# Optimization experiments

Hardware: AMD Instinct MI355X
Metric: run time of the kernel (lower is better)

Reference implementation:

```python
import jax, jax.numpy as jnp
import numpy as np

EMBED = 1024
N_HEAD = 16
D_HID = EMBED // N_HEAD
R_FF = 4
D_FF = EMBED * R_FF
LN_EPS = 1e-5


def layer_norm(x, gamma, beta):
    mu = jnp.mean(x, axis=-1, keepdims=True)
    var = jnp.var(x, axis=-1, keepdims=True)
    return (x - mu) * jax.lax.rsqrt(var + LN_EPS) * gamma + beta


def setup_inputs() -> dict:
    key = jax.random.key(0)
    ks = jax.random.split(key, 10)
    B, S = 4, 2048
    # torch nn.Linear stores weight as [out, in]; y = x @ W.T
    def xavier(k, shape):
        fan_out, fan_in = shape
        lim = np.sqrt(6.0 / (fan_in + fan_out))
        return jax.random.uniform(k, shape, jnp.float32, -lim, lim)
    return {
        "x": jax.random.normal(ks[0], (B, S, EMBED), jnp.float32),
        "Wq": xavier(ks[1], (EMBED, EMBED)),
        "Wk": xavier(ks[2], (EMBED, EMBED)),
        "Wv": xavier(ks[3], (EMBED, EMBED)),
        "Wo": xavier(ks[4], (EMBED, EMBED)),
        "bo": jnp.zeros((EMBED,), jnp.float32),
        "ln1_g": jnp.ones((EMBED,), jnp.float32),
        "ln1_b": jnp.zeros((EMBED,), jnp.float32),
        "ln2_g": jnp.ones((EMBED,), jnp.float32),
        "ln2_b": jnp.zeros((EMBED,), jnp.float32),
        "W1": jax.random.normal(ks[5], (D_FF, EMBED), jnp.float32) * np.sqrt(2.0 / EMBED),
        "b1": jnp.zeros((D_FF,), jnp.float32),
        "W2": xavier(ks[6], (EMBED, D_FF)),
        "b2": jnp.zeros((EMBED,), jnp.float32),
    }


def reference(x, Wq, Wk, Wv, Wo, bo, ln1_g, ln1_b, ln2_g, ln2_b, W1, b1, W2, b2):
    B, S, E = x.shape
    scaling = 1.0 / np.sqrt(D_HID)
    # --- attention (pre-LN), dropout = identity (eval) ---
    xn = layer_norm(x, ln1_g, ln1_b)
    q = (xn @ Wq.T).reshape(B, S, N_HEAD, D_HID) * scaling
    k = (xn @ Wk.T).reshape(B, S, N_HEAD, D_HID)
    v = (xn @ Wv.T).reshape(B, S, N_HEAD, D_HID)
    scores = jnp.einsum("bqhd,bkhd->bhqk", q, k)
    attn = jax.nn.softmax(scores, axis=-1)
    out = jnp.einsum("bhqk,bkhd->bqhd", attn, v).reshape(B, S, E)
    out = out @ Wo.T + bo
    x = x + out
    # --- feed-forward (pre-LN) ---
    xn = layer_norm(x, ln2_g, ln2_b)
    h = jax.nn.relu(xn @ W1.T + b1)
    x = x + (h @ W2.T + b2)
    return x
```

## Files before the change

kernel.cpp:

```cpp
#include <hip/hip_runtime.h>
#include <hip/hip_bf16.h>
#include <cstdint>


typedef __attribute__((ext_vector_type(8))) short bf16x8;
typedef __attribute__((ext_vector_type(4))) float f32x4;

#define LDSAS __attribute__((address_space(3)))
#define GLBAS __attribute__((address_space(1)))

#define CQK 0.18033688011112044f

__device__ __forceinline__ unsigned short f2bf(float f) {
  union { float f; unsigned u; } c; c.f = f;
  unsigned u = c.u + 0x7fffu + ((c.u >> 16) & 1u);
  return (unsigned short)(u >> 16);
}

__device__ __forceinline__ unsigned pk2(float a, float b) {
  __hip_bfloat162 h = __float22bfloat162_rn(make_float2(a, b));
  union { __hip_bfloat162 h; unsigned u; } c; c.h = h; return c.u;
}

__device__ __forceinline__ void async16(const unsigned short* g, unsigned short* l) {
  __builtin_amdgcn_global_load_lds((const GLBAS unsigned int*)g,
                                   (LDSAS unsigned int*)l, 16, 0, 0);
}

__global__ void cvt_all(const float* __restrict__ q, const float* __restrict__ k,
                        const float* __restrict__ v, const float* __restrict__ o,
                        const float* __restrict__ w1, const float* __restrict__ w2,
                        unsigned short* __restrict__ wsb) {
  const long i = (long)blockIdx.x * 256 + threadIdx.x;
  const float* src; unsigned short* dst; long off;
  if (i < 1048576) {
    const long seg = i >> 18, o4 = i & 262143;
    src = (seg == 0) ? q : (seg == 1) ? k : (seg == 2) ? v : o;
    dst = wsb + ((seg == 3) ? 3145728L : seg * 1048576L);
    off = o4;
  } else if (i < 2097152) {
    src = w1; dst = wsb + 4194304; off = i - 1048576;
  } else {
    src = w2; dst = wsb + 8388608; off = i - 2097152;
  }
  const float4 vv = ((const float4*)src)[off];
  ushort4 r;
  r.x = f2bf(vv.x); r.y = f2bf(vv.y); r.z = f2bf(vv.z); r.w = f2bf(vv.w);
  ((ushort4*)dst)[off] = r;
}

__global__ void ln_fwd(const float* __restrict__ x, const float* __restrict__ g,
                       const float* __restrict__ bb, unsigned short* __restrict__ outp) {
  const int row = blockIdx.x, tid = threadIdx.x;
  const float4 v = ((const float4*)(x + (long)row * 1024))[tid];
  float s  = v.x + v.y + v.z + v.w;
  float sq = v.x * v.x + v.y * v.y + v.z * v.z + v.w * v.w;
#pragma unroll
  for (int off = 1; off < 64; off <<= 1) {
    s  += __shfl_xor(s, off);
    sq += __shfl_xor(sq, off);
  }
  __shared__ float red[8];
  const int wv = tid >> 6, lane = tid & 63;
  if (lane == 0) { red[wv] = s; red[4 + wv] = sq; }
  __syncthreads();
  s  = red[0] + red[1] + red[2] + red[3];
  sq = red[4] + red[5] + red[6] + red[7];
  const float mu  = s * (1.f / 1024.f);
  const float var = sq * (1.f / 1024.f) - mu * mu;
  const float rstd = rsqrtf(var + 1e-5f);
  const float4 gv = ((const float4*)g)[tid];
  const float4 bv = ((const float4*)bb)[tid];
  ushort4 o;
  o.x = f2bf((v.x - mu) * rstd * gv.x + bv.x);
  o.y = f2bf((v.y - mu) * rstd * gv.y + bv.y);
  o.z = f2bf((v.z - mu) * rstd * gv.z + bv.z);
  o.w = f2bf((v.w - mu) * rstd * gv.w + bv.w);
  ((ushort4*)(outp + (long)row * 1024))[tid] = o;
}

template <int EPI>
__launch_bounds__(256, 3)
__global__ void gemm_bt(const unsigned short* __restrict__ A,
                        const unsigned short* __restrict__ B,
                        void* __restrict__ Cout,
                        const float* __restrict__ bias,
                        const float* __restrict__ res,
                        int M, int N, int K) {
  __shared__ __align__(16) unsigned short As[128 * 64];
  __shared__ __align__(16) unsigned short Bs[128 * 64];
  const int tid  = threadIdx.x;
  const int lane = tid & 63;
  const int wvu  = __builtin_amdgcn_readfirstlane(tid >> 6);
  const int quad = lane >> 4, l16 = lane & 15;
  const int wm = wvu >> 1, wn = wvu & 1;

  const int gx = gridDim.x;
  const int id = blockIdx.y * gx + blockIdx.x;
  const int xcd = id & 7, slot = id >> 3;
  const int by = xcd * 8 + (slot & 7);
  const int bx = slot >> 3;
  const long m0 = (long)by * 128, n0 = (long)bx * 128;

  f32x4 acc[4][4];
#pragma unroll
  for (int i = 0; i < 4; i++)
#pragma unroll
    for (int j = 0; j < 4; j++) acc[i][j] = (f32x4){0.f, 0.f, 0.f, 0.f};

  const int rxA = l16 & 7;
  const int c0A = quad ^ rxA;
  int srow[4], sgc[4];
#pragma unroll
  for (int j = 0; j < 4; ++j) {
    const int s = wvu * 256 + j * 64 + lane;
    srow[j] = s >> 3;
    sgc[j] = ((s & 7) ^ (srow[j] & 7)) * 8;
  }

  for (int k0 = 0; k0 < K; k0 += 64) {
    __syncthreads();
#pragma unroll
    for (int j = 0; j < 4; ++j) {
      const int db = (wvu * 256 + j * 64) * 8;
      async16(A + (m0 + srow[j]) * K + k0 + sgc[j], As + db);
      async16(B + (n0 + srow[j]) * K + k0 + sgc[j], Bs + db);
    }
    __syncthreads();

#pragma unroll
    for (int kc = 0; kc < 2; ++kc) {
      const int ch = (c0A ^ (kc * 4)) * 8;
      bf16x8 af[4], bfr[4];
#pragma unroll
      for (int t = 0; t < 4; ++t) {
        af[t]  = *(const bf16x8*)(As + (wm * 64 + t * 16 + l16) * 64 + ch);
        bfr[t] = *(const bf16x8*)(Bs + (wn * 64 + t * 16 + l16) * 64 + ch);
      }
#pragma unroll
      for (int mt = 0; mt < 4; ++mt)
#pragma unroll
        for (int nt = 0; nt < 4; ++nt)
          acc[mt][nt] = __builtin_amdgcn_mfma_f32_16x16x32_bf16(af[mt], bfr[nt],
                                                                acc[mt][nt], 0, 0, 0);
    }
  }

#pragma unroll
  for (int nt = 0; nt < 4; ++nt) {
    const long col = n0 + wn * 64 + nt * 16 + l16;
    float bv = 0.f;
    if (EPI == 1 || EPI == 2) bv = bias[col];
    const float scl = (EPI == 3 && col < 1024) ? CQK : 1.0f;
#pragma unroll
    for (int mt = 0; mt < 4; ++mt) {
#pragma unroll
      for (int r = 0; r < 4; ++r) {
        const long row = m0 + wm * 64 + mt * 16 + quad * 4 + r;
        const long idx = row * (long)N + col;
        float v = acc[mt][nt][r];
        if (EPI == 0) {
          ((unsigned short*)Cout)[idx] = f2bf(v);
        } else if (EPI == 1) {
          ((float*)Cout)[idx] = v + bv + res[idx];
        } else if (EPI == 2) {
          v += bv;
          ((unsigned short*)Cout)[idx] = f2bf(v > 0.f ? v : 0.f);
        } else {
          ((unsigned short*)Cout)[idx] = f2bf(v * scl);
        }
      }
    }
  }
}

#define LDA4(AF, BUF, H)                                                        \
  do {                                                                          \
    const unsigned short* _p = As + ((BUF) * 2 + (H)) * 8192;                   \
    _Pragma("unroll") for (int _m = 0; _m < 4; ++_m) {                          \
      AF[_m][0] = *(const bf16x8*)(_p + (_m * 32 + rA) * 64 + chk0);            \
      AF[_m][1] = *(const bf16x8*)(_p + (_m * 32 + rA) * 64 + chk1);            \
    }                                                                           \
  } while (0)

#define LDB2(BF, BUF, H)                                                        \
  do {                                                                          \
    const unsigned short* _p = Bs + ((BUF) * 2 + (H)) * 8192;                   \
    _Pragma("unroll") for (int _n = 0; _n < 2; ++_n) {                          \
      BF[_n][0] = *(const bf16x8*)(_p + (_n * 64 + rB) * 64 + chk0);            \
      BF[_n][1] = *(const bf16x8*)(_p + (_n * 64 + rB) * 64 + chk1);            \
    }                                                                           \
  } while (0)

#define MFMA8(MB, NB, AF, BF)                                                   \
  do {                                                                          \
    _Pragma("unroll") for (int _m = 0; _m < 4; ++_m)                            \
    _Pragma("unroll") for (int _n = 0; _n < 2; ++_n) {                          \
      acc[(MB) + _m][(NB) + _n] = __builtin_amdgcn_mfma_f32_16x16x32_bf16(      \
          AF[_m][0], BF[_n][0], acc[(MB) + _m][(NB) + _n], 0, 0, 0);            \
      acc[(MB) + _m][(NB) + _n] = __builtin_amdgcn_mfma_f32_16x16x32_bf16(      \
          AF[_m][1], BF[_n][1], acc[(MB) + _m][(NB) + _n], 0, 0, 0);            \
    }                                                                           \
  } while (0)

#define PH_MID()                                                                \
  __builtin_amdgcn_s_barrier();                                                 \
  asm volatile("s_waitcnt lgkmcnt(0)" ::: "memory");                            \
  __builtin_amdgcn_sched_barrier(0);                                            \
  __builtin_amdgcn_s_setprio(1)

#define PH_END()                                                                \
  __builtin_amdgcn_s_setprio(0);                                                \
  __builtin_amdgcn_sched_barrier(0);                                            \
  __builtin_amdgcn_s_barrier();                                                 \
  __builtin_amdgcn_sched_barrier(0)

template <int EPI>
__launch_bounds__(512, 2)
__global__ void gemm256(const unsigned short* __restrict__ A,
                        const unsigned short* __restrict__ B,
                        void* __restrict__ Cout,
                        const float* __restrict__ bias,
                        int M, int N, int K) {
  extern __shared__ __align__(16) unsigned short lds[];
  unsigned short* As = lds;
  unsigned short* Bs = lds + 32768;

  const int tid  = threadIdx.x;
  const int lane = tid & 63;
  const int wv   = __builtin_amdgcn_readfirstlane(tid >> 6);
  const int quad = lane >> 4, l16 = lane & 15;
  const int wm = wv >> 2, wn = wv & 3;

  const int id = blockIdx.x;
  const int xcd = id & 7, slot = id >> 3;
  const int by = xcd * 4 + (slot & 3);
  const int bx = slot >> 2;
  const long m0 = (long)by * 256, n0 = (long)bx * 256;

  const int s0 = wv * 64 + lane;
  const int r0 = s0 >> 3;
  const int c0 = (s0 ^ r0) & 7;
  const int s1 = 512 + s0;
  const int r1 = s1 >> 3;
  const int c1 = (s1 ^ r1) & 7;
  const long rt0 = (long)r0 * K + c0 * 8;
  const long rt1 = (long)r1 * K + c1 * 8;
  const unsigned short* Ab = A + m0 * K;
  const unsigned short* Bb = B + n0 * K;

  const int rA = wm * 16 + l16;
  const int rB = wn * 16 + l16;
  const int chk0 = (quad ^ (l16 & 7)) * 8;
  const int chk1 = chk0 ^ 32;

  f32x4 acc[8][4];
#pragma unroll
  for (int a_ = 0; a_ < 8; ++a_)
#pragma unroll
    for (int b_ = 0; b_ < 4; ++b_) acc[a_][b_] = (f32x4){0.f, 0.f, 0.f, 0.f};

  auto stgA = [&](int b, int h, long kk) {
    const unsigned short* s = Ab + (long)h * 128 * K + kk;
    unsigned short* d = As + (b * 2 + h) * 8192 + wv * 512;
    async16(s + rt0, d);
    async16(s + rt1, d + 4096);
  };
  auto stgB = [&](int b, int h, long kk) {
    const unsigned short* s = Bb + (long)h * 128 * K + kk;
    unsigned short* d = Bs + (b * 2 + h) * 8192 + wv * 512;
    async16(s + rt0, d);
    async16(s + rt1, d + 4096);
  };

  stgA(0, 0, 0); stgA(0, 1, 0); stgB(0, 0, 0); stgB(0, 1, 0);
  stgB(1, 0, 64); stgA(1, 0, 64); stgB(1, 1, 64);
  asm volatile("s_waitcnt vmcnt(6)" ::: "memory");
  __builtin_amdgcn_s_barrier();
  __builtin_amdgcn_sched_barrier(0);

  const int NI = K >> 7;
  for (int it = 0; it < NI; ++it) {
    const long kt  = (long)it * 128;
    const long ku  = kt + 64;
    const long kt2 = kt + 128;
    const long kt3 = kt + 192;
    const bool more = (it + 1 < NI);

    bf16x8 bq[2][2];
    {
      bf16x8 a[4][2];
      LDA4(a, 0, 0); LDB2(bq, 0, 0);
      stgA(1, 1, ku);
      PH_MID();
      MFMA8(0, 0, a, bq);
      PH_END();
    }
    {
      bf16x8 a[4][2];
      LDA4(a, 0, 1);
      if (more) stgB(0, 0, kt2);
      PH_MID();
      MFMA8(4, 0, a, bq);
      PH_END();
    }
    {
      bf16x8 a[4][2];
      LDA4(a, 0, 0); LDB2(bq, 0, 1);
      PH_MID();
      MFMA8(0, 2, a, bq);
      PH_END();
    }
    {
      bf16x8 a[4][2];
      LDA4(a, 0, 1);
      if (more) { stgA(0, 0, kt2); stgB(0, 1, kt2); }
      PH_MID();
      MFMA8(4, 2, a, bq);
      __builtin_amdgcn_s_setprio(0);
      __builtin_amdgcn_sched_barrier(0);
      if (more) { asm volatile("s_waitcnt vmcnt(6)" ::: "memory"); }
      else      { asm volatile("s_waitcnt vmcnt(0)" ::: "memory"); }
      __builtin_amdgcn_s_barrier();
      __builtin_amdgcn_sched_barrier(0);
    }
    {
      bf16x8 a[4][2];
      LDA4(a, 1, 0); LDB2(bq, 1, 0);
      if (more) stgA(0, 1, kt2);
      PH_MID();
      MFMA8(0, 0, a, bq);
      PH_END();
    }
    {
      bf16x8 a[4][2];
      LDA4(a, 1, 1);
      if (more) stgB(1, 0, kt3);
      PH_MID();
      MFMA8(4, 0, a, bq);
      PH_END();
    }
    {
      bf16x8 a[4][2];
      LDA4(a, 1, 0); LDB2(bq, 1, 1);
      PH_MID();
      MFMA8(0, 2, a, bq);
      PH_END();
    }
    {
      bf16x8 a[4][2];
      LDA4(a, 1, 1);
      if (more) { stgA(1, 0, kt3); stgB(1, 1, kt3); }
      PH_MID();
      MFMA8(4, 2, a, bq);
      __builtin_amdgcn_s_setprio(0);
      __builtin_amdgcn_sched_barrier(0);
      if (more) { asm volatile("s_waitcnt vmcnt(6)" ::: "memory"); }
      __builtin_amdgcn_s_barrier();
      __builtin_amdgcn_sched_barrier(0);
    }
  }

#pragma unroll
  for (int nt = 0; nt < 4; ++nt) {
    const long col = n0 + nt * 64 + wn * 16 + l16;
    const float bv = (EPI == 2) ? bias[col] : 0.f;
    const float scl = (EPI == 3 && col < 1024) ? CQK : 1.0f;
#pragma unroll
    for (int mt = 0; mt < 8; ++mt) {
#pragma unroll
      for (int r = 0; r < 4; ++r) {
        const long row = m0 + mt * 32 + wm * 16 + quad * 4 + r;
        const long idx = row * (long)N + col;
        float v = acc[mt][nt][r];
        if (EPI == 2) {
          v += bv;
          ((unsigned short*)Cout)[idx] = f2bf(v > 0.f ? v : 0.f);
        } else {
          ((unsigned short*)Cout)[idx] = f2bf(v * scl);
        }
      }
    }
  }
}

__global__ void vprep(const unsigned short* __restrict__ qkv,
                      unsigned short* __restrict__ vt) {
  __shared__ unsigned short T[64 * 68];
  const int tid = threadIdx.x;
  const int t = blockIdx.x;
  const int bh = blockIdx.y;
  const int b = bh >> 4, h = bh & 15;
  const long base = ((long)b * 2048 + t * 64) * 3072 + 2048 + h * 64;
#pragma unroll
  for (int i = 0; i < 4; ++i) {
    int c = i * 256 + tid;
    int r = c >> 4, d4 = (c & 15) * 4;
    *(ushort4*)(T + r * 68 + d4) = *(const ushort4*)(qkv + base + (long)r * 3072 + d4);
  }
  __syncthreads();
  unsigned short* out = vt + ((long)bh * 32 + t) * 4096;
#pragma unroll
  for (int i = 0; i < 4; ++i) {
    int u = i * 256 + tid;
    int c = u >> 1, half = u & 1;
    int d = c >> 3;
    int k = ((c & 7) - d) & 7;
    int kvp4 = k * 8 + half * 4;
    int sk = (kvp4 & 32) | ((kvp4 & 4) << 2) | ((kvp4 & 16) >> 1) | ((kvp4 & 8) >> 1);
    ushort4 o;
    o.x = T[(sk + 0) * 68 + d];
    o.y = T[(sk + 1) * 68 + d];
    o.z = T[(sk + 2) * 68 + d];
    o.w = T[(sk + 3) * 68 + d];
    *(ushort4*)(out + u * 4) = o;
  }
}

__launch_bounds__(256, 3)
__global__ void attn_fwd(const unsigned short* __restrict__ qkv,
                         const unsigned short* __restrict__ vt,
                         unsigned short* __restrict__ outp) {
  __shared__ __align__(16) unsigned short Qs[128 * 64];
  __shared__ __align__(16) unsigned short Ks[128 * 64];
  __shared__ __align__(16) unsigned short Vs[128 * 64];

  const int tid = threadIdx.x;
  const int lane = tid & 63;
  const int wv = __builtin_amdgcn_readfirstlane(tid >> 6);
  const int quad = lane >> 4, l16 = lane & 15;

  const int id = blockIdx.y * 16 + blockIdx.x;
  const int xcd = id & 7, slot = id >> 3;
  const int bh = xcd * 8 + (slot >> 4);
  const int qt = slot & 15;
  const int b = bh >> 4, h = bh & 15;
  const long rowbase = (long)b * 2048;
  const int hoff = h * 64;

  {
    const unsigned short* qsrc = qkv + (rowbase + qt * 128) * 3072 + hoff;
#pragma unroll
    for (int j = 0; j < 4; ++j) {
      const int c = j * 256 + wv * 64 + lane;
      const int row = c >> 3;
      const int k = ((c & 7) - row) & 7;
      async16(qsrc + (long)row * 3072 + k * 8, Qs + (j * 256 + wv * 64) * 8);
    }
  }
  __syncthreads();

  const int rot0 = (quad + l16) & 7;
  const int rot1 = rot0 ^ 4;

  bf16x8 bq[2][2];
#pragma unroll
  for (int s = 0; s < 2; ++s) {
    const int qrow = wv * 32 + s * 16 + l16;
    bq[s][0] = *(const bf16x8*)(Qs + qrow * 64 + rot0 * 8);
    bq[s][1] = *(const bf16x8*)(Qs + qrow * 64 + rot1 * 8);
  }

  const int c0 = wv * 64 + lane;
  const int r0 = c0 >> 3;
  const int ks = ((c0 & 7) - r0) & 7;
  const unsigned short* kptr = qkv + (rowbase + r0) * 3072 + 1024 + hoff + ks * 8;
  const unsigned short* vptr = vt + (long)bh * 131072 + (long)c0 * 8;
  unsigned short* kdst = Ks + wv * 512;
  unsigned short* vdst = Vs + wv * 512;

  bf16x8 ones;
#pragma unroll
  for (int i = 0; i < 8; ++i) ones[i] = (short)0x3F80;

  f32x4 oacc[2][4], lacc[2];
#pragma unroll
  for (int s = 0; s < 2; ++s) {
    lacc[s] = (f32x4){0.f, 0.f, 0.f, 0.f};
#pragma unroll
    for (int i = 0; i < 4; ++i) oacc[s][i] = (f32x4){0.f, 0.f, 0.f, 0.f};
  }

  for (int kt = 0; kt < 16; ++kt) {
    __syncthreads();
#pragma unroll
    for (int j = 0; j < 4; ++j) {
      async16(kptr + (long)j * 32 * 3072, kdst + j * 2048);
      async16(vptr + j * 2048, vdst + j * 2048);
    }
    kptr += (long)128 * 3072;
    vptr += 8192;
    __syncthreads();

    f32x4 sacc[2][8];
#pragma unroll
    for (int t = 0; t < 8; ++t) {
      const int ar = t * 16 + l16;
      bf16x8 ak0 = *(const bf16x8*)(Ks + ar * 64 + rot0 * 8);
      bf16x8 ak1 = *(const bf16x8*)(Ks + ar * 64 + rot1 * 8);
#pragma unroll
      for (int s = 0; s < 2; ++s) {
        f32x4 z = (f32x4){0.f, 0.f, 0.f, 0.f};
        z = __builtin_amdgcn_mfma_f32_16x16x32_bf16(ak0, bq[s][0], z, 0, 0, 0);
        sacc[s][t] = __builtin_amdgcn_mfma_f32_16x16x32_bf16(ak1, bq[s][1], z, 0, 0, 0);
      }
    }

    union APU { unsigned u[4]; bf16x8 v; } ap[2][4];
#pragma unroll
    for (int s = 0; s < 2; ++s)
#pragma unroll
      for (int hf = 0; hf < 4; ++hf) {
#pragma unroll
        for (int t = 0; t < 2; ++t) {
          const f32x4 sv = sacc[s][hf * 2 + t];
          const float p0 = __builtin_amdgcn_exp2f(sv[0]);
          const float p1 = __builtin_amdgcn_exp2f(sv[1]);
          const float p2 = __builtin_amdgcn_exp2f(sv[2]);
          const float p3 = __builtin_amdgcn_exp2f(sv[3]);
          ap[s][hf].u[t * 2 + 0] = pk2(p0, p1);
          ap[s][hf].u[t * 2 + 1] = pk2(p2, p3);
        }
        lacc[s] = __builtin_amdgcn_mfma_f32_16x16x32_bf16(ap[s][hf].v, ones,
                                                          lacc[s], 0, 0, 0);
      }

#pragma unroll
    for (int hf = 0; hf < 4; ++hf) {
      const int vbase = (hf >> 1) * 4096 + ((hf & 1) ? rot1 : rot0) * 8;
#pragma unroll
      for (int dt = 0; dt < 4; ++dt) {
        bf16x8 bv = *(const bf16x8*)(Vs + vbase + (dt * 16 + l16) * 64);
#pragma unroll
        for (int s = 0; s < 2; ++s)
          oacc[s][dt] = __builtin_amdgcn_mfma_f32_16x16x32_bf16(ap[s][hf].v, bv,
                                                                oacc[s][dt], 0, 0, 0);
      }
    }
  }

#pragma unroll
  for (int s = 0; s < 2; ++s) {
    float linv[4];
#pragma unroll
    for (int r = 0; r < 4; ++r) linv[r] = 1.f / lacc[s][r];
#pragma unroll
    for (int dt = 0; dt < 4; ++dt)
#pragma unroll
      for (int r = 0; r < 4; ++r) {
        const long row = rowbase + qt * 128 + wv * 32 + s * 16 + quad * 4 + r;
        outp[row * 1024 + hoff + dt * 16 + l16] = f2bf(oacc[s][dt][r] * linv[r]);
      }
  }
}

extern "C" void kernel_launch(void* const* d_in, const int* in_sizes, int n_in,
                              void* d_out, int out_size, void* d_ws, size_t ws_size,
                              hipStream_t stream) {
  (void)in_sizes; (void)n_in; (void)out_size; (void)ws_size;
  const float* x   = (const float*)d_in[0];
  const float* Wq  = (const float*)d_in[1];
  const float* Wk  = (const float*)d_in[2];
  const float* Wv  = (const float*)d_in[3];
  const float* Wo  = (const float*)d_in[4];
  const float* bo  = (const float*)d_in[5];
  const float* g1  = (const float*)d_in[6];
  const float* be1 = (const float*)d_in[7];
  const float* g2  = (const float*)d_in[8];
  const float* be2 = (const float*)d_in[9];
  const float* W1  = (const float*)d_in[10];
  const float* bf1 = (const float*)d_in[11];
  const float* W2  = (const float*)d_in[12];
  const float* bf2 = (const float*)d_in[13];

  static bool s_attr = false;
  if (!s_attr) {
    hipFuncSetAttribute(reinterpret_cast<const void*>(&gemm256<3>),
                        hipFuncAttributeMaxDynamicSharedMemorySize, 131072);
    hipFuncSetAttribute(reinterpret_cast<const void*>(&gemm256<2>),
                        hipFuncAttributeMaxDynamicSharedMemorySize, 131072);
    s_attr = true;
  }

  char* ws = (char*)d_ws;
  unsigned short* wqkv  = (unsigned short*)(ws);
  unsigned short* wo    = (unsigned short*)(ws + 6291456);
  unsigned short* w1    = (unsigned short*)(ws + 8388608);
  unsigned short* w2    = (unsigned short*)(ws + 16777216);
  unsigned short* xn    = (unsigned short*)(ws + 25165824);
  unsigned short* big   = (unsigned short*)(ws + 41943040);
  unsigned short* attnb = (unsigned short*)(ws + 109051904);
  float*          x1    = (float*)(ws + 125829120);
  unsigned short* vtg   = xn;

  cvt_all<<<12288, 256, 0, stream>>>(Wq, Wk, Wv, Wo, W1, W2, wqkv);

  ln_fwd<<<8192, 256, 0, stream>>>(x, g1, be1, xn);
  gemm256<3><<<dim3(384), 512, 131072, stream>>>(xn, wqkv, big, nullptr,
                                                 8192, 3072, 1024);
  vprep<<<dim3(32, 64), 256, 0, stream>>>(big, vtg);
  attn_fwd<<<dim3(16, 64), 256, 0, stream>>>(big, vtg, attnb);
  gemm_bt<1><<<dim3(8, 64), 256, 0, stream>>>(attnb, wo, x1, bo, x,
                                              8192, 1024, 1024);
  ln_fwd<<<8192, 256, 0, stream>>>(x1, g2, be2, xn);
  gemm256<2><<<dim3(512), 512, 131072, stream>>>(xn, w1, big, bf1,
                                                 8192, 4096, 1024);
  gemm_bt<1><<<dim3(8, 64), 256, 0, stream>>>(big, w2, (float*)d_out, bf2, x1,
                                              8192, 1024, 4096);
}
```

Measured before the change: 488.0 us.

## Reorder GEMM subtile phases in a snake pattern to reuse LDS fragments

The 256x256 GEMM main loop now walks its four quadrant phases in a serpentine order (0,0 → 0,2 → 4,2 → 4,0), so each phase reuses either the A or the B register fragment from the previous one. This removes two of the four A-tile LDS reloads per half-iteration. The global-to-LDS staging order for A and B halves is also rearranged to match the new consumption order. This raises register pressure because A and B fragments are held across phases, and the staging order must still respect the buffer reuse guarded by the waits and barriers.

```diff
diff --git a/kernel.cpp b/kernel.cpp
--- a/kernel.cpp
+++ b/kernel.cpp
@@ -273,8 +273,8 @@
     async16(s + rt1, d + 4096);
   };
 
-  stgA(0, 0, 0); stgA(0, 1, 0); stgB(0, 0, 0); stgB(0, 1, 0);
-  stgB(1, 0, 64); stgA(1, 0, 64); stgB(1, 1, 64);
+  stgA(0, 0, 0); stgB(0, 1, 0); stgA(0, 1, 0); stgB(0, 0, 0);
+  stgA(1, 0, 64); stgB(1, 1, 64); stgA(1, 1, 64);
   asm volatile("s_waitcnt vmcnt(6)" ::: "memory");
   __builtin_amdgcn_s_barrier();
   __builtin_amdgcn_sched_barrier(0);
@@ -287,36 +287,27 @@
     const long kt3 = kt + 192;
     const bool more = (it + 1 < NI);
 
-    bf16x8 bq[2][2];
     {
-      bf16x8 a[4][2];
-      LDA4(a, 0, 0); LDB2(bq, 0, 0);
-      stgA(1, 1, ku);
-      PH_MID();
-      MFMA8(0, 0, a, bq);
+      bf16x8 a0[4][2], a1[4][2], b0[2][2], b1[2][2];
+      LDA4(a0, 0, 0); LDB2(b0, 0, 0);
+      stgB(1, 0, ku);
+      PH_MID();
+      MFMA8(0, 0, a0, b0);
       PH_END();
-    }
-    {
-      bf16x8 a[4][2];
-      LDA4(a, 0, 1);
-      if (more) stgB(0, 0, kt2);
-      PH_MID();
-      MFMA8(4, 0, a, bq);
+      LDB2(b1, 0, 1);
+      if (more) stgA(0, 0, kt2);
+      PH_MID();
+      MFMA8(0, 2, a0, b1);
       PH_END();
-    }
-    {
-      bf16x8 a[4][2];
-      LDA4(a, 0, 0); LDB2(bq, 0, 1);
-      PH_MID();
-      MFMA8(0, 2, a, bq);
+      LDA4(a1, 0, 1);
+      if (more) stgB(0, 1, kt2);
+      PH_MID();
+      MFMA8(4, 2, a1, b1);
       PH_END();
-    }
-    {
-      bf16x8 a[4][2];
-      LDA4(a, 0, 1);
-      if (more) { stgA(0, 0, kt2); stgB(0, 1, kt2); }
-      PH_MID();
-      MFMA8(4, 2, a, bq);
+      LDB2(b0, 0, 0);
+      if (more) stgA(0, 1, kt2);
+      PH_MID();
+      MFMA8(4, 0, a1, b0);
       __builtin_amdgcn_s_setprio(0);
       __builtin_amdgcn_sched_barrier(0);
       if (more) { asm volatile("s_waitcnt vmcnt(6)" ::: "memory"); }
@@ -325,34 +316,26 @@
       __builtin_amdgcn_sched_barrier(0);
     }
     {
-      bf16x8 a[4][2];
-      LDA4(a, 1, 0); LDB2(bq, 1, 0);
-      if (more) stgA(0, 1, kt2);
-      PH_MID();
-      MFMA8(0, 0, a, bq);
+      bf16x8 a0[4][2], a1[4][2], b0[2][2], b1[2][2];
+      LDA4(a0, 1, 0); LDB2(b0, 1, 0);
+      if (more) stgB(0, 0, kt2);
+      PH_MID();
+      MFMA8(0, 0, a0, b0);
       PH_END();
-    }
-    {
-      bf16x8 a[4][2];
-      LDA4(a, 1, 1);
-      if (more) stgB(1, 0, kt3);
-      PH_MID();
-      MFMA8(4, 0, a, bq);
+      LDB2(b1, 1, 1);
+      if (more) stgA(1, 0, kt3);
+      PH_MID();
+      MFMA8(0, 2, a0, b1);
       PH_END();
-    }
-    {
-      bf16x8 a[4][2];
-      LDA4(a, 1, 0); LDB2(bq, 1, 1);
-      PH_MID();
-      MFMA8(0, 2, a, bq);
+      LDA4(a1, 1, 1);
+      if (more) stgB(1, 1, kt3);
+      PH_MID();
+      MFMA8(4, 2, a1, b1);
       PH_END();
-    }
-    {
-      bf16x8 a[4][2];
-      LDA4(a, 1, 1);
-      if (more) { stgA(1, 0, kt3); stgB(1, 1, kt3); }
-      PH_MID();
-      MFMA8(4, 2, a, bq);
+      LDB2(b0, 1, 0);
+      if (more) stgA(1, 1, kt3);
+      PH_MID();
+      MFMA8(4, 0, a1, b0);
       __builtin_amdgcn_s_setprio(0);
       __builtin_amdgcn_sched_barrier(0);
       if (more) { asm volatile("s_waitcnt vmcnt(6)" ::: "memory"); }
```

Result: faster. 472.4 us (-3.2%).
